# Optimization experiments

Measured on AMD Instinct MI355X. Metric: run time of the kernel, lower is better.

The kernel has to match this reference:

```python
import jax, jax.numpy as jnp
import numpy as np

N, E, B = 50000, 800000, 64
DIN, H, NH, L = 128, 128, 4, 3
SYM = 64          # symbolic_feature_dim
FD, ED = SYM // 4, H // 4   # feature_dim=16, embed_dim=32
DH = H // NH
EPS = 1e-5

def _ln(x, g, b):
    m = jnp.mean(x, -1, keepdims=True)
    v = jnp.var(x, -1, keepdims=True)
    return (x - m) * jax.lax.rsqrt(v + EPS) * g + b

def setup_inputs() -> dict:
    key = jax.random.key(0)
    ks = jax.random.split(key, 32)
    s = 0.05
    inp = {
        'node_features': jax.random.normal(ks[0], (N, DIN), jnp.float32),
        'symbolic_features': jax.random.normal(ks[1], (B, SYM), jnp.float32),
        'edge_index': jax.random.randint(ks[2], (2, E), 0, N),
        'batch': jnp.sort(jax.random.randint(ks[3], (N,), 0, B)),
        # GraphEncoder params
        'W_in': jax.random.normal(ks[4], (H, DIN)) * s,
        'b_in': jnp.zeros((H,)),
        'sage_Wl': jax.random.normal(ks[5], (L, H, H)) * s,   # lin_l (neighbors, with bias)
        'sage_bl': jnp.zeros((L, H)),
        'sage_Wr': jax.random.normal(ks[6], (L, H, H)) * s,   # lin_r (root, no bias)
        'ln_g': jnp.ones((L, H)), 'ln_b': jnp.zeros((L, H)),
        # AttentionPooling params
        'query': jax.random.normal(ks[7], (H,)),
        'in_proj_W': jax.random.normal(ks[8], (3 * H, H)) * s,
        'in_proj_b': jnp.zeros((3 * H,)),
        'out_W': jax.random.normal(ks[9], (H, H)) * s,
        'out_b': jnp.zeros((H,)),
        # SymbolicFeatureProcessor params (4 stacked encoders)
        'sym_W': jax.random.normal(ks[10], (4, ED, FD)) * s,
        'sym_b': jnp.zeros((4, ED)),
        'symf_W': jax.random.normal(ks[11], (H, H)) * s,
        'symf_b': jnp.zeros((H,)),
        'symf_g': jnp.ones((H,)), 'symf_beta': jnp.zeros((H,)),
        # main fusion
        'fus_W': jax.random.normal(ks[12], (H, 2 * H)) * s,
        'fus_b': jnp.zeros((H,)),
        'fus_g': jnp.ones((H,)), 'fus_beta': jnp.zeros((H,)),
        # 3 output heads stacked (instability, grounding, risk)
        'head_W1': jax.random.normal(ks[13], (3, H // 2, H)) * s,
        'head_b1': jnp.zeros((3, H // 2)),
        'head_W2': jax.random.normal(ks[14], (3, 1, H // 2)) * s,
        'head_b2': jnp.zeros((3, 1)),
    }
    return inp

def reference(node_features, symbolic_features, W_in, b_in, sage_Wl, sage_bl, sage_Wr,
              ln_g, ln_b, query, in_proj_W, in_proj_b, out_W, out_b,
              sym_W, sym_b, symf_W, symf_b, symf_g, symf_beta,
              fus_W, fus_b, fus_g, fus_beta, head_W1, head_b1, head_W2, head_b2,
              edge_index, batch):
    src, dst = edge_index[0], edge_index[1]
    x = jax.nn.relu(node_features @ W_in.T + b_in)                 # [N,H]
    deg = jax.ops.segment_sum(jnp.ones((E, 1), x.dtype), dst, num_segments=N)
    inv_deg = 1.0 / jnp.maximum(deg, 1.0)
    for l in range(L):
        res = x
        agg = jax.ops.segment_sum(x[src], dst, num_segments=N) * inv_deg  # mean aggr
        h = agg @ sage_Wl[l].T + sage_bl[l] + x @ sage_Wr[l].T
        x = jax.nn.relu(_ln(h, ln_g[l], ln_b[l])) + res
    # ---- AttentionPooling: per-graph MHA with a single learned query ----
    Wq, Wk, Wv = jnp.split(in_proj_W, 3, axis=0)
    bq, bk, bv = jnp.split(in_proj_b, 3)
    q = (Wq @ query + bq).reshape(NH, DH)                          # [NH,DH]
    k = (x @ Wk.T + bk).reshape(N, NH, DH)
    v = (x @ Wv.T + bv).reshape(N, NH, DH)
    scores = jnp.einsum('nhd,hd->nh', k, q) / np.sqrt(DH)          # [N,NH]
    smax = jax.ops.segment_max(scores, batch, num_segments=B)      # [B,NH]
    e = jnp.exp(scores - smax[batch])
    den = jax.ops.segment_sum(e, batch, num_segments=B)
    w = e / den[batch]                                              # segment softmax
    pooled = jax.ops.segment_sum(w[:, :, None] * v, batch, num_segments=B)
    g = pooled.reshape(B, H) @ out_W.T + out_b                      # [B,H]
    # ---- SymbolicFeatureProcessor: 4 parallel encoders + fusion ----
    parts = symbolic_features.reshape(B, 4, FD)
    emb = jax.nn.relu(jnp.einsum('bfi,foi->bfo', parts, sym_W) + sym_b)  # [B,4,ED]
    sym = _ln(jax.nn.relu(emb.reshape(B, H) @ symf_W.T + symf_b), symf_g, symf_beta)
    # ---- Fusion + heads ----
    fused = _ln(jax.nn.relu(jnp.concatenate([g, sym], -1) @ fus_W.T + fus_b), fus_g, fus_beta)
    hh = jax.nn.relu(jnp.einsum('bi,koi->kbo', fused, head_W1) + head_b1[:, None, :])
    out = jax.nn.sigmoid(jnp.einsum('kbo,kpo->kbp', hh, head_W2) + head_b2[:, None, :])
    return (out[0], out[1], out[2])
```

## Files before the change

### kernel.cpp

```cpp
#include <hip/hip_runtime.h>


#define H 128
#define PPG 16
#define BKSH 8
#define CH 4096

typedef unsigned short u16;
typedef unsigned char u8;
typedef __attribute__((ext_vector_type(8))) short bf16x8;
typedef __attribute__((ext_vector_type(4))) float f32x4;

__device__ __forceinline__ float b2f(u16 u){ return __uint_as_float(((unsigned)u) << 16); }
__device__ __forceinline__ u16 f2b(float f){
    unsigned x = __float_as_uint(f);
    unsigned r = x + 0x7fffu + ((x >> 16) & 1u);
    return (u16)(r >> 16);
}
__device__ __forceinline__ unsigned enc4(float v){
    int n = (int)(fmaxf(v, 0.f) * (15.f / 7.f) + 0.5f);
    return (unsigned)min(n, 15);
}
__device__ __forceinline__ unsigned pk_fp4(const float* nv){
    unsigned r = 0;
    #pragma unroll
    for (int j = 0; j < 8; j++) r |= enc4(nv[j]) << (4 * j);
    return r;
}
__device__ __forceinline__ void acc_lin4(unsigned* ua, unsigned w){
    ua[0] += w & 0x000F000Fu;
    ua[1] += (w >> 4) & 0x000F000Fu;
    ua[2] += (w >> 8) & 0x000F000Fu;
    ua[3] += (w >> 12) & 0x000F000Fu;
}
__device__ __forceinline__ void lds_fence(){
    asm volatile("s_waitcnt lgkmcnt(0)" ::: "memory");
    __builtin_amdgcn_sched_barrier(0);
}

__global__ __launch_bounds__(256) void k_splitall(const float* __restrict__ W_in, const float* __restrict__ sWl,
                                                  const float* __restrict__ sWr, const float* __restrict__ ipW,
                                                  u16* __restrict__ Win, u16* __restrict__ Wl,
                                                  u16* __restrict__ Wr, u16* __restrict__ Wv){
    const int WSZ = H * H;
    int i = blockIdx.x * 256 + threadIdx.x;
    if (i < WSZ)               Win[i]           = f2b(W_in[i]);
    else if (i < 4 * WSZ)      Wl[i - WSZ]      = f2b(sWl[i - WSZ]);
    else if (i < 7 * WSZ)      Wr[i - 4 * WSZ]  = f2b(sWr[i - 4 * WSZ]);
    else if (i < 8 * WSZ)      Wv[i - 7 * WSZ]  = f2b(ipW[2 * WSZ + (i - 7 * WSZ)]);
}

__global__ __launch_bounds__(1024) void k_bcnt(const int* __restrict__ dst, int* __restrict__ bcnt,
                                               int E, int NBK){
    __shared__ int cnt[256];
    int tid = threadIdx.x;
    if (tid < 256) cnt[tid] = 0;
    __syncthreads();
    int e0 = blockIdx.x * CH;
    int n = min(CH, E - e0);
    for (int j = tid; j < n; j += 1024) atomicAdd(&cnt[dst[e0 + j] >> BKSH], 1);
    __syncthreads();
    if (tid < NBK && cnt[tid]) atomicAdd(&bcnt[tid], cnt[tid]);
}

__global__ __launch_bounds__(256) void k_bscan(const int* __restrict__ bcnt, int* __restrict__ boff,
                                               int* __restrict__ bcur, int* __restrict__ offs, int NBK, int N){
    __shared__ int pre[256];
    int tid = threadIdx.x;
    int v = (tid < NBK) ? bcnt[tid] : 0;
    pre[tid] = v;
    __syncthreads();
    for (int off = 1; off < 256; off <<= 1){
        int a = (tid >= off) ? pre[tid - off] : 0;
        __syncthreads();
        pre[tid] += a;
        __syncthreads();
    }
    int excl = pre[tid] - v;
    if (tid < NBK){ boff[tid] = excl; bcur[tid] = excl; }
    if (tid == 255){
        boff[NBK] = pre[255];
        offs[N] = pre[255];
    }
}

__global__ __launch_bounds__(1024) void k_bscatter(const int* __restrict__ src, const int* __restrict__ dst,
                                                   unsigned* __restrict__ ebuf, int* __restrict__ bcur,
                                                   int E, int NBK){
    __shared__ int cnt[256], pre[256], loc[256], lcur[256], base[256];
    __shared__ unsigned stage[CH];
    int tid = threadIdx.x;
    if (tid < 256){ cnt[tid] = 0; }
    __syncthreads();
    int e0 = blockIdx.x * CH;
    int n = min(CH, E - e0);
    for (int j = tid; j < n; j += 1024) atomicAdd(&cnt[dst[e0 + j] >> BKSH], 1);
    __syncthreads();
    if (tid < NBK) base[tid] = atomicAdd(&bcur[tid], cnt[tid]);
    if (tid < 256) pre[tid] = cnt[tid];
    __syncthreads();
    for (int off = 1; off < 256; off <<= 1){
        int v = (tid < 256 && tid >= off) ? pre[tid - off] : 0;
        __syncthreads();
        if (tid < 256) pre[tid] += v;
        __syncthreads();
    }
    if (tid < 256){ loc[tid] = pre[tid] - cnt[tid]; lcur[tid] = loc[tid]; }
    __syncthreads();
    for (int j = tid; j < n; j += 1024){
        int d = dst[e0 + j], s = src[e0 + j];
        int k = d >> BKSH;
        int p = atomicAdd(&lcur[k], 1);
        stage[p] = (unsigned)d | ((unsigned)s << 16);
    }
    __syncthreads();
    for (int j = tid; j < n; j += 1024){
        unsigned v = stage[j];
        int k = (v & 0xffffu) >> BKSH;
        ebuf[base[k] + (j - loc[k])] = v;
    }
}

__global__ __launch_bounds__(256) void k_bfill(const unsigned* __restrict__ ebuf, const int* __restrict__ boff,
                                               int* __restrict__ offs, int* __restrict__ csr,
                                               float* __restrict__ invdeg, int N){
    __shared__ int deg[256], pre[256], cur[256];
    int k = blockIdx.x, tid = threadIdx.x;
    int node0 = k << BKSH;
    int s0 = boff[k], s1 = boff[k + 1];
    deg[tid] = 0;
    __syncthreads();
    for (int j = s0 + tid; j < s1; j += 256) atomicAdd(&deg[ebuf[j] & 255u], 1);
    __syncthreads();
    pre[tid] = deg[tid];
    __syncthreads();
    for (int off = 1; off < 256; off <<= 1){
        int v = (tid >= off) ? pre[tid - off] : 0;
        __syncthreads();
        pre[tid] += v;
        __syncthreads();
    }
    int excl = pre[tid] - deg[tid];
    int node = node0 + tid;
    if (node < N){
        offs[node] = s0 + excl;
        invdeg[node] = 1.0f / (float)max(deg[tid], 1);
    }
    cur[tid] = s0 + excl;
    __syncthreads();
    for (int j = s0 + tid; j < s1; j += 256){
        unsigned v = ebuf[j];
        int p = atomicAdd(&cur[v & 255u], 1);
        csr[p] = (int)(v >> 16);
    }
}

__global__ void k_start(const int* __restrict__ batch, int* __restrict__ start, int N, int B){
    int n = blockIdx.x * blockDim.x + threadIdx.x;
    if (n >= N) return;
    int b = batch[n];
    int bp = (n == 0) ? -1 : batch[n - 1];
    for (int g = bp + 1; g <= b; g++) start[g] = n;
    if (n == N - 1){ for (int g = b + 1; g <= B; g++) start[g] = N; }
}

__global__ __launch_bounds__(256) void k_gemm0(const float* __restrict__ A, u16* __restrict__ Xb,
                                               u8* __restrict__ X4,
                                               const u16* __restrict__ W1, const float* __restrict__ bias,
                                               int nrows){
    __shared__ float lt[4][16 * 132];
    const int wave = threadIdx.x >> 6;
    const int l = threadIdx.x & 63;
    const int q = l >> 4;
    const int t = l & 15;
    const int row0 = blockIdx.x * 64 + wave * 16;

    u16* sw = (u16*)&lt[wave][0];
    #pragma unroll
    for (int i = 0; i < 8; i++){
        int p = (i * 64 + l) * 4;
        int row = p >> 7, col = p & 127;
        int rowg = min(row0 + row, nrows - 1);
        float4 v = *(const float4*)(A + (size_t)rowg * H + col);
        u16* d = sw + row * 136 + col;
        d[0] = f2b(v.x); d[1] = f2b(v.y); d[2] = f2b(v.z); d[3] = f2b(v.w);
    }
    lds_fence();
    bf16x8 a1[4];
    #pragma unroll
    for (int kk = 0; kk < 4; kk++)
        a1[kk] = *(const bf16x8*)(sw + t * 136 + q * 8 + kk * 32);
    lds_fence();

    f32x4 acc[8];
    #pragma unroll
    for (int nt = 0; nt < 8; nt++){
        f32x4 c = {0.f, 0.f, 0.f, 0.f};
        const size_t wof = (size_t)(nt * 16 + t) * H + q * 8;
        #pragma unroll
        for (int kk = 0; kk < 4; kk++)
            c = __builtin_amdgcn_mfma_f32_16x16x32_bf16(a1[kk], *(const bf16x8*)(W1 + wof + kk * 32), c, 0, 0, 0);
        acc[nt] = c;
    }
    float bv[8];
    #pragma unroll
    for (int nt = 0; nt < 8; nt++) bv[nt] = bias[nt * 16 + t];
    #pragma unroll
    for (int r = 0; r < 4; r++)
        #pragma unroll
        for (int nt = 0; nt < 8; nt++)
            lt[wave][(q * 4 + r) * 132 + nt * 16 + t] = fmaxf(acc[nt][r] + bv[nt], 0.f);
    lds_fence();
    #pragma unroll
    for (int i = 0; i < 4; i++){
        int p = (i * 64 + l) * 8;
        int row = p >> 7, col = p & 127;
        int rg = row0 + row;
        if (rg < nrows){
            const float* lp = &lt[wave][row * 132 + col];
            float4 v0 = *(const float4*)lp;
            float4 v1 = *(const float4*)(lp + 4);
            float nv[8] = {v0.x, v0.y, v0.z, v0.w, v1.x, v1.y, v1.z, v1.w};
            bf16x8 o;
            #pragma unroll
            for (int j = 0; j < 8; j++) o[j] = (short)f2b(nv[j]);
            *(bf16x8*)(Xb + (size_t)rg * H + col) = o;
            int q4 = (col & 31) >> 3, kk4 = col >> 5;
            *(unsigned*)(X4 + (size_t)rg * 64 + q4 * 16 + kk4 * 4) = pk_fp4(nv);
        }
    }
}

template<bool FSC>
__global__ __launch_bounds__(128) void k_layer(
    const u16* __restrict__ Xin, const u8* __restrict__ Xin4,
    u16* __restrict__ Xout, u8* __restrict__ Xout4,
    const int* __restrict__ offs, const int* __restrict__ csr, const float* __restrict__ invdeg,
    const u16* __restrict__ W1, const u16* __restrict__ W2,
    const float* __restrict__ bias, const float* __restrict__ lng, const float* __restrict__ lnb,
    u16* __restrict__ Vb, const u16* __restrict__ Wv, const float* __restrict__ vbias,
    const float* __restrict__ qk, const float* __restrict__ qkb, float* __restrict__ scores,
    int nrows)
{
    __shared__ float ltw[16 * 132];
    __shared__ u16 sx[16 * 136];
    const int wave = threadIdx.x >> 6;
    const int l = threadIdx.x & 63;
    const int q = l >> 4;
    const int t = l & 15;
    const int row0g = blockIdx.x * 16;
    const int myrow = row0g + t;
    const bool valid = myrow < nrows;

    #pragma unroll
    for (int i = 0; i < 2; i++){
        int p = (i * 128 + threadIdx.x) * 8;
        int row = p >> 7, col = p & 127;
        int rowg = min(row0g + row, nrows - 1);
        uint4 v = *(const uint4*)(Xin + (size_t)rowg * H + col);
        *(uint4*)(sx + row * 136 + col) = v;
    }
    __syncthreads();
    bf16x8 a2[4];
    if (wave == 0){
        #pragma unroll
        for (int kk = 0; kk < 4; kk++)
            a2[kk] = *(const bf16x8*)(sx + t * 136 + q * 8 + kk * 32);
    }
    unsigned ua[4][4];
    #pragma unroll
    for (int kk = 0; kk < 4; kk++)
        #pragma unroll
        for (int m = 0; m < 4; m++) ua[kk][m] = 0u;
    int o0 = valid ? offs[myrow] : 0;
    int o1 = valid ? offs[myrow + 1] : 0;
    int mid = o0 + ((o1 - o0 + 1) >> 1);
    int i  = wave ? mid : o0;
    int ie = wave ? o1 : mid;
    int p0 = 0, p1 = 0, p2 = 0, p3 = 0;
    if (i + 3 < ie){ p0 = csr[i]; p1 = csr[i + 1]; p2 = csr[i + 2]; p3 = csr[i + 3]; }
    while (i + 3 < ie){
        int t0 = p0, t1 = p1, t2 = p2, t3 = p3;
        int nx = i + 4;
        if (nx + 3 < ie){ p0 = csr[nx]; p1 = csr[nx + 1]; p2 = csr[nx + 2]; p3 = csr[nx + 3]; }
        uint4 w0 = *(const uint4*)(Xin4 + (size_t)t0 * 64 + q * 16);
        uint4 w1 = *(const uint4*)(Xin4 + (size_t)t1 * 64 + q * 16);
        uint4 w2 = *(const uint4*)(Xin4 + (size_t)t2 * 64 + q * 16);
        uint4 w3 = *(const uint4*)(Xin4 + (size_t)t3 * 64 + q * 16);
        acc_lin4(ua[0], w0.x); acc_lin4(ua[1], w0.y); acc_lin4(ua[2], w0.z); acc_lin4(ua[3], w0.w);
        acc_lin4(ua[0], w1.x); acc_lin4(ua[1], w1.y); acc_lin4(ua[2], w1.z); acc_lin4(ua[3], w1.w);
        acc_lin4(ua[0], w2.x); acc_lin4(ua[1], w2.y); acc_lin4(ua[2], w2.z); acc_lin4(ua[3], w2.w);
        acc_lin4(ua[0], w3.x); acc_lin4(ua[1], w3.y); acc_lin4(ua[2], w3.z); acc_lin4(ua[3], w3.w);
        i = nx;
    }
    for (; i < ie; i++){
        int s = csr[i];
        uint4 w = *(const uint4*)(Xin4 + (size_t)s * 64 + q * 16);
        acc_lin4(ua[0], w.x); acc_lin4(ua[1], w.y); acc_lin4(ua[2], w.z); acc_lin4(ua[3], w.w);
    }
    if (wave == 1){
        unsigned* pw = (unsigned*)(ltw + t * 132) + q * 16;
        #pragma unroll
        for (int kk = 0; kk < 4; kk++)
            #pragma unroll
            for (int m = 0; m < 4; m++) pw[kk * 4 + m] = ua[kk][m];
    }
    __syncthreads();
    if (wave == 1) return;
    {
        const unsigned* pr = (const unsigned*)(ltw + t * 132) + q * 16;
        #pragma unroll
        for (int kk = 0; kk < 4; kk++)
            #pragma unroll
            for (int m = 0; m < 4; m++) ua[kk][m] += pr[kk * 4 + m];
    }
    lds_fence();
    float scl = (valid ? invdeg[myrow] : 0.f) * (7.f / 15.f);
    bf16x8 a1[4];
    #pragma unroll
    for (int kk = 0; kk < 4; kk++){
        bf16x8 v;
        #pragma unroll
        for (int m = 0; m < 4; m++){
            v[m]     = (short)f2b((float)(ua[kk][m] & 0xFFFFu) * scl);
            v[m + 4] = (short)f2b((float)(ua[kk][m] >> 16) * scl);
        }
        a1[kk] = v;
    }

    f32x4 acc[8];
    #pragma unroll
    for (int nt = 0; nt < 8; nt++){
        f32x4 c = {0.f, 0.f, 0.f, 0.f};
        const size_t wof = (size_t)(nt * 16 + t) * H + q * 8;
        #pragma unroll
        for (int kk = 0; kk < 4; kk++)
            c = __builtin_amdgcn_mfma_f32_16x16x32_bf16(a1[kk], *(const bf16x8*)(W1 + wof + kk * 32), c, 0, 0, 0);
        #pragma unroll
        for (int kk = 0; kk < 4; kk++)
            c = __builtin_amdgcn_mfma_f32_16x16x32_bf16(a2[kk], *(const bf16x8*)(W2 + wof + kk * 32), c, 0, 0, 0);
        acc[nt] = c;
    }
    float bv[8], gv[8], lbv[8];
    #pragma unroll
    for (int nt = 0; nt < 8; nt++){
        int col = nt * 16 + t;
        bv[nt] = bias[col]; gv[nt] = lng[col]; lbv[nt] = lnb[col];
    }
    #pragma unroll
    for (int r = 0; r < 4; r++){
        float hv[8], s = 0.f, s2 = 0.f;
        #pragma unroll
        for (int nt = 0; nt < 8; nt++){ float v = acc[nt][r] + bv[nt]; hv[nt] = v; s += v; s2 += v * v; }
        #pragma unroll
        for (int m = 1; m < 16; m <<= 1){ s += __shfl_xor(s, m, 64); s2 += __shfl_xor(s2, m, 64); }
        float mean = s * (1.f / H);
        float var  = s2 * (1.f / H) - mean * mean;
        float rstd = rsqrtf(var + 1e-5f);
        #pragma unroll
        for (int nt = 0; nt < 8; nt++){
            float v = (hv[nt] - mean) * rstd * gv[nt] + lbv[nt];
            ltw[(q * 4 + r) * 132 + nt * 16 + t] = fmaxf(v, 0.f);
        }
    }
    lds_fence();
    if (!FSC){
        #pragma unroll
        for (int i2 = 0; i2 < 4; i2++){
            int p = (i2 * 64 + l) * 8;
            int row = p >> 7, col = p & 127;
            int rg = row0g + row;
            if (rg < nrows){
                const float* lp = ltw + row * 132 + col;
                float4 v0 = *(const float4*)lp;
                float4 v1 = *(const float4*)(lp + 4);
                const u16* xp = sx + row * 136 + col;
                float nv[8];
                nv[0] = v0.x + b2f(xp[0]); nv[1] = v0.y + b2f(xp[1]);
                nv[2] = v0.z + b2f(xp[2]); nv[3] = v0.w + b2f(xp[3]);
                nv[4] = v1.x + b2f(xp[4]); nv[5] = v1.y + b2f(xp[5]);
                nv[6] = v1.z + b2f(xp[6]); nv[7] = v1.w + b2f(xp[7]);
                bf16x8 o;
                #pragma unroll
                for (int j = 0; j < 8; j++) o[j] = (short)f2b(nv[j]);
                *(bf16x8*)(Xout + (size_t)rg * H + col) = o;
                int q4 = (col & 31) >> 3, kk4 = col >> 5;
                *(unsigned*)(Xout4 + (size_t)rg * 64 + q4 * 16 + kk4 * 4) = pk_fp4(nv);
            }
        }
    } else {
        bf16x8 xv[4];
        float sc[4] = {0.f, 0.f, 0.f, 0.f};
        #pragma unroll
        for (int kk = 0; kk < 4; kk++){
            const float* lp = ltw + t * 132 + q * 8 + kk * 32;
            float4 v0 = *(const float4*)lp;
            float4 v1 = *(const float4*)(lp + 4);
            float nv[8] = {v0.x, v0.y, v0.z, v0.w, v1.x, v1.y, v1.z, v1.w};
            #pragma unroll
            for (int j = 0; j < 8; j++) nv[j] += b2f((u16)a2[kk][j]);
            bf16x8 o;
            #pragma unroll
            for (int j = 0; j < 8; j++) o[j] = (short)f2b(nv[j]);
            xv[kk] = o;
            #pragma unroll
            for (int h = 0; h < 4; h++){
                const float* qp = qk + h * H + q * 8 + kk * 32;
                float4 q0 = *(const float4*)qp;
                float4 q1 = *(const float4*)(qp + 4);
                sc[h] += nv[0] * q0.x + nv[1] * q0.y + nv[2] * q0.z + nv[3] * q0.w
                       + nv[4] * q1.x + nv[5] * q1.y + nv[6] * q1.z + nv[7] * q1.w;
            }
        }
        #pragma unroll
        for (int h = 0; h < 4; h++){
            sc[h] += __shfl_xor(sc[h], 16, 64);
            sc[h] += __shfl_xor(sc[h], 32, 64);
        }
        if (q == 0 && valid){
            #pragma unroll
            for (int h = 0; h < 4; h++) scores[myrow * 4 + h] = sc[h] + qkb[h];
        }
        f32x4 vacc[8];
        #pragma unroll
        for (int nt = 0; nt < 8; nt++){
            f32x4 c = {0.f, 0.f, 0.f, 0.f};
            const size_t wof = (size_t)(nt * 16 + t) * H + q * 8;
            #pragma unroll
            for (int kk = 0; kk < 4; kk++)
                c = __builtin_amdgcn_mfma_f32_16x16x32_bf16(xv[kk], *(const bf16x8*)(Wv + wof + kk * 32), c, 0, 0, 0);
            vacc[nt] = c;
        }
        float vb2[8];
        #pragma unroll
        for (int nt = 0; nt < 8; nt++) vb2[nt] = vbias[nt * 16 + t];
        #pragma unroll
        for (int r = 0; r < 4; r++)
            #pragma unroll
            for (int nt = 0; nt < 8; nt++)
                ltw[(q * 4 + r) * 132 + nt * 16 + t] = vacc[nt][r] + vb2[nt];
        lds_fence();
        #pragma unroll
        for (int i2 = 0; i2 < 4; i2++){
            int p = (i2 * 64 + l) * 8;
            int row = p >> 7, col = p & 127;
            int rg = row0g + row;
            if (rg < nrows){
                const float* lp = ltw + row * 132 + col;
                float4 v0 = *(const float4*)lp;
                float4 v1 = *(const float4*)(lp + 4);
                bf16x8 o;
                o[0] = (short)f2b(v0.x); o[1] = (short)f2b(v0.y);
                o[2] = (short)f2b(v0.z); o[3] = (short)f2b(v0.w);
                o[4] = (short)f2b(v1.x); o[5] = (short)f2b(v1.y);
                o[6] = (short)f2b(v1.z); o[7] = (short)f2b(v1.w);
                *(bf16x8*)(Vb + (size_t)rg * H + col) = o;
            }
        }
    }
}

__global__ __launch_bounds__(128) void k_qk(const float* __restrict__ ipW, const float* __restrict__ ipb,
                                            const float* __restrict__ query,
                                            float* __restrict__ qk, float* __restrict__ qkb){
    __shared__ float qs[H];
    int t = threadIdx.x;
    float a = ipb[t];
    for (int c = 0; c < H; c++) a += ipW[t * H + c] * query[c];
    qs[t] = a;
    __syncthreads();
    const float r32 = 0.17677669529663687f;
    #pragma unroll
    for (int h = 0; h < 4; h++){
        float v = 0.f;
        for (int d = 0; d < 32; d++) v += ipW[(H + h * 32 + d) * H + t] * qs[h * 32 + d];
        qk[h * H + t] = v * r32;
    }
    if (t < 4){
        float z = 0.f;
        for (int d = 0; d < 32; d++) z += ipb[H + t * 32 + d] * qs[t * 32 + d];
        qkb[t] = z * r32;
    }
}

__global__ __launch_bounds__(256) void k_smax(const float* __restrict__ scores, const int* __restrict__ start,
                                              float* __restrict__ smax, int B){
    int idx = blockIdx.x * 4 + (threadIdx.x >> 6);
    if (idx >= B * 4) return;
    int b = idx >> 2, h = idx & 3, l = threadIdx.x & 63;
    int s0 = start[b], s1 = start[b + 1];
    float m = -1e30f;
    for (int n = s0 + l; n < s1; n += 64) m = fmaxf(m, scores[n * 4 + h]);
    #pragma unroll
    for (int s = 1; s < 64; s <<= 1) m = fmaxf(m, __shfl_xor(m, s, 64));
    if (l == 0) smax[idx] = m;
}

__global__ __launch_bounds__(64) void k_poolsum(const float* __restrict__ scores, const u16* __restrict__ Vb,
                                                const int* __restrict__ start, const float* __restrict__ smax,
                                                float* __restrict__ praw, float* __restrict__ den){
    int b = blockIdx.x / PPG, p = blockIdx.x % PPG;
    int c2 = threadIdx.x;
    int h = c2 >> 4;
    int s0 = start[b], s1 = start[b + 1];
    float sm = smax[b * 4 + h];
    float a0 = 0.f, a1 = 0.f, se = 0.f;
    for (int n = s0 + p; n < s1; n += PPG){
        float e = expf(scores[n * 4 + h] - sm);
        unsigned wv = *(const unsigned*)(Vb + (size_t)n * H + 2 * c2);
        a0 += e * b2f((u16)(wv & 0xffffu));
        a1 += e * b2f((u16)(wv >> 16));
        se += e;
    }
    atomicAdd(&praw[b * H + 2 * c2], a0);
    atomicAdd(&praw[b * H + 2 * c2 + 1], a1);
    if ((c2 & 15) == 0) atomicAdd(&den[b * 4 + h], se);
}

__global__ __launch_bounds__(128) void k_tail(
    const float* __restrict__ praw, const float* __restrict__ den,
    const float* __restrict__ outW, const float* __restrict__ outb,
    const float* __restrict__ symfeat, const float* __restrict__ symW, const float* __restrict__ symb,
    const float* __restrict__ sfW, const float* __restrict__ sfb, const float* __restrict__ sfg, const float* __restrict__ sfbeta,
    const float* __restrict__ fusW, const float* __restrict__ fusb, const float* __restrict__ fusg, const float* __restrict__ fusbeta,
    const float* __restrict__ hW1, const float* __restrict__ hb1, const float* __restrict__ hW2, const float* __restrict__ hb2,
    float* __restrict__ dout, int B){
    int b = blockIdx.x, t = threadIdx.x;
    __shared__ float P[H], G[H], EMB[H], S[H], F[H], HHs[192], red[H], mm[2];
    float dh = den[b * 4 + (t >> 5)];
    P[t] = (dh > 0.f) ? praw[b * H + t] / dh : 0.f;
    __syncthreads();
    float a = outb[t];
    for (int c = 0; c < H; c++) a += P[c] * outW[t * H + c];
    G[t] = a;
    {
        int f = t >> 5;
        float e = symb[t];
        for (int i = 0; i < 16; i++) e += symfeat[b * 64 + f * 16 + i] * symW[t * 16 + i];
        EMB[t] = fmaxf(e, 0.f);
    }
    __syncthreads();
    float a2 = sfb[t];
    for (int c = 0; c < H; c++) a2 += EMB[c] * sfW[t * H + c];
    a2 = fmaxf(a2, 0.f);
    red[t] = a2; __syncthreads();
    for (int s = 64; s > 0; s >>= 1){ if (t < s) red[t] += red[t + s]; __syncthreads(); }
    if (t == 0) mm[0] = red[0];
    __syncthreads();
    red[t] = a2 * a2; __syncthreads();
    for (int s = 64; s > 0; s >>= 1){ if (t < s) red[t] += red[t + s]; __syncthreads(); }
    if (t == 0) mm[1] = red[0];
    __syncthreads();
    {
        float mean = mm[0] * (1.f / H), var = mm[1] * (1.f / H) - mean * mean;
        float rstd = rsqrtf(var + 1e-5f);
        S[t] = (a2 - mean) * rstd * sfg[t] + sfbeta[t];
    }
    __syncthreads();
    float fu = fusb[t];
    for (int c = 0; c < H; c++) fu += G[c] * fusW[t * 256 + c];
    for (int c = 0; c < H; c++) fu += S[c] * fusW[t * 256 + 128 + c];
    fu = fmaxf(fu, 0.f);
    red[t] = fu; __syncthreads();
    for (int s = 64; s > 0; s >>= 1){ if (t < s) red[t] += red[t + s]; __syncthreads(); }
    if (t == 0) mm[0] = red[0];
    __syncthreads();
    red[t] = fu * fu; __syncthreads();
    for (int s = 64; s > 0; s >>= 1){ if (t < s) red[t] += red[t + s]; __syncthreads(); }
    if (t == 0) mm[1] = red[0];
    __syncthreads();
    {
        float mean = mm[0] * (1.f / H), var = mm[1] * (1.f / H) - mean * mean;
        float rstd = rsqrtf(var + 1e-5f);
        F[t] = (fu - mean) * rstd * fusg[t] + fusbeta[t];
    }
    __syncthreads();
    for (int idx = t; idx < 192; idx += 128){
        float hv = hb1[idx];
        for (int c = 0; c < H; c++) hv += F[c] * hW1[idx * H + c];
        HHs[idx] = fmaxf(hv, 0.f);
    }
    __syncthreads();
    if (t < 3){
        float z = hb2[t];
        for (int o = 0; o < 64; o++) z += HHs[t * 64 + o] * hW2[t * 64 + o];
        dout[t * B + b] = 1.f / (1.f + expf(-z));
    }
}

extern "C" void kernel_launch(void* const* d_in, const int* in_sizes, int n_in,
                              void* d_out, int out_size, void* d_ws, size_t ws_size,
                              hipStream_t stream){
    const float* NF      = (const float*)d_in[0];
    const float* SYMF    = (const float*)d_in[1];
    const int*   EIDX    = (const int*)d_in[2];
    const int*   BATCH   = (const int*)d_in[3];
    const float* W_in    = (const float*)d_in[4];
    const float* b_in    = (const float*)d_in[5];
    const float* sWl     = (const float*)d_in[6];
    const float* sbl     = (const float*)d_in[7];
    const float* sWr     = (const float*)d_in[8];
    const float* lng     = (const float*)d_in[9];
    const float* lnb     = (const float*)d_in[10];
    const float* query   = (const float*)d_in[11];
    const float* ipW     = (const float*)d_in[12];
    const float* ipb     = (const float*)d_in[13];
    const float* outW    = (const float*)d_in[14];
    const float* outb    = (const float*)d_in[15];
    const float* symW    = (const float*)d_in[16];
    const float* symb    = (const float*)d_in[17];
    const float* sfW     = (const float*)d_in[18];
    const float* sfb     = (const float*)d_in[19];
    const float* sfg     = (const float*)d_in[20];
    const float* sfbeta  = (const float*)d_in[21];
    const float* fusW    = (const float*)d_in[22];
    const float* fusb    = (const float*)d_in[23];
    const float* fusg    = (const float*)d_in[24];
    const float* fusbeta = (const float*)d_in[25];
    const float* hW1     = (const float*)d_in[26];
    const float* hb1     = (const float*)d_in[27];
    const float* hW2     = (const float*)d_in[28];
    const float* hb2     = (const float*)d_in[29];

    const int N = in_sizes[0] / H;
    const int E = in_sizes[2] / 2;
    const int B = in_sizes[1] / 64;
    const int* esrc = EIDX;
    const int* edst = EIDX + E;
    const int NBK = (N + 255) >> BKSH;

    char* w = (char*)d_ws;
    auto alloc = [&](size_t bytes) -> char* {
        char* p = w; w += (bytes + 255) & ~(size_t)255; return p;
    };
    u16*   X0      = (u16*)alloc((size_t)N * H * 2);
    u16*   X1      = (u16*)alloc((size_t)N * H * 2);
    u8*    X0q     = (u8*)alloc((size_t)N * 64);
    u8*    X1q     = (u8*)alloc((size_t)N * 64);
    u16*   Vb      = (u16*)alloc((size_t)N * H * 2);
    float* scores  = (float*)alloc((size_t)N * 4 * 4);
    unsigned* ebuf = (unsigned*)alloc((size_t)E * 4);
    char* zbase    = w;
    int* bcnt      = (int*)alloc((size_t)NBK * 4);
    float* praw    = (float*)alloc((size_t)B * H * 4);
    float* den     = (float*)alloc((size_t)B * 4 * 4);
    size_t zbytes  = (size_t)(w - zbase);
    int* boff      = (int*)alloc((size_t)(NBK + 1) * 4);
    int* bcur      = (int*)alloc((size_t)NBK * 4);
    int* offs      = (int*)alloc((size_t)(N + 1) * 4);
    float* invdeg  = (float*)alloc((size_t)N * 4);
    int* csr       = (int*)alloc((size_t)E * 4);
    int* start     = (int*)alloc((size_t)(B + 1) * 4);
    float* smax    = (float*)alloc((size_t)B * 4 * 4);
    float* qk      = (float*)alloc((size_t)4 * H * 4);
    float* qkb     = (float*)alloc(4 * 4);
    const int WSZ  = H * H;
    u16* Win = (u16*)alloc(WSZ * 2);
    u16* Wl  = (u16*)alloc(3 * WSZ * 2);
    u16* Wr  = (u16*)alloc(3 * WSZ * 2);
    u16* Wv  = (u16*)alloc(WSZ * 2);

    hipMemsetAsync(zbase, 0, zbytes, stream);

    const int cb = (E + CH - 1) / CH;
    k_bcnt<<<cb, 1024, 0, stream>>>(edst, bcnt, E, NBK);
    k_bscan<<<1, 256, 0, stream>>>(bcnt, boff, bcur, offs, NBK, N);
    k_bscatter<<<cb, 1024, 0, stream>>>(esrc, edst, ebuf, bcur, E, NBK);
    k_bfill<<<NBK, 256, 0, stream>>>(ebuf, boff, offs, csr, invdeg, N);
    k_start<<<(N + 255) / 256, 256, 0, stream>>>(BATCH, start, N, B);
    k_qk<<<1, 128, 0, stream>>>(ipW, ipb, query, qk, qkb);
    k_splitall<<<(8 * WSZ + 255) / 256, 256, 0, stream>>>(W_in, sWl, sWr, ipW, Win, Wl, Wr, Wv);

    const int gb = (N + 63) / 64;
    const int lb = (N + 15) / 16;
    k_gemm0<<<gb, 256, 0, stream>>>(NF, X0, X0q, Win, b_in, N);
    k_layer<false><<<lb, 128, 0, stream>>>(X0, X0q, X1, X1q, offs, csr, invdeg,
                                           Wl + 0 * WSZ, Wr + 0 * WSZ,
                                           sbl + 0 * H, lng + 0 * H, lnb + 0 * H,
                                           nullptr, nullptr, nullptr,
                                           nullptr, nullptr, nullptr, N);
    k_layer<false><<<lb, 128, 0, stream>>>(X1, X1q, X0, X0q, offs, csr, invdeg,
                                           Wl + 1 * WSZ, Wr + 1 * WSZ,
                                           sbl + 1 * H, lng + 1 * H, lnb + 1 * H,
                                           nullptr, nullptr, nullptr,
                                           nullptr, nullptr, nullptr, N);
    k_layer<true><<<lb, 128, 0, stream>>>(X0, X0q, nullptr, nullptr, offs, csr, invdeg,
                                          Wl + 2 * WSZ, Wr + 2 * WSZ,
                                          sbl + 2 * H, lng + 2 * H, lnb + 2 * H,
                                          Vb, Wv, ipb + 2 * H,
                                          qk, qkb, scores, N);
    k_smax<<<B, 256, 0, stream>>>(scores, start, smax, B);
    k_poolsum<<<B * PPG, 64, 0, stream>>>(scores, Vb, start, smax, praw, den);
    k_tail<<<B, 128, 0, stream>>>(praw, den, outW, outb, SYMF, symW, symb,
                                  sfW, sfb, sfg, sfbeta, fusW, fusb, fusg, fusbeta,
                                  hW1, hb1, hW2, hb2, (float*)d_out, B);
}
```

Measured before the change: 364.3 us.

## Merge prep kernels, store attention values as fp8, use shuffle reductions in tail

Four small setup kernels (bucket count, graph start offsets, query-key projection, weight conversion) are folded into one block-specialized prep launch, which removes launch overhead. The attention value matrix V is now stored as fp8 instead of bf16, halving its write and read traffic in the last layer and in pooling. The pooling kernel is restructured so each lane decodes four values and the two half-waves are combined with a shuffle. The tail kernel's LDS tree reductions are replaced with wave shuffles. The fp8 values reduce the precision of the pooled result.

```diff
diff --git a/kernel.cpp b/kernel.cpp
--- a/kernel.cpp
+++ b/kernel.cpp
@@ -10,6 +10,7 @@
 typedef unsigned char u8;
 typedef __attribute__((ext_vector_type(8))) short bf16x8;
 typedef __attribute__((ext_vector_type(4))) float f32x4;
+typedef __attribute__((ext_vector_type(2))) float f32x2;
 
 __device__ __forceinline__ float b2f(u16 u){ return __uint_as_float(((unsigned)u) << 16); }
 __device__ __forceinline__ u16 f2b(float f){
@@ -21,7 +22,7 @@
     int n = (int)(fmaxf(v, 0.f) * (15.f / 7.f) + 0.5f);
     return (unsigned)min(n, 15);
 }
-__device__ __forceinline__ unsigned pk_fp4(const float* nv){
+__device__ __forceinline__ unsigned pk_lin4(const float* nv){
     unsigned r = 0;
     #pragma unroll
     for (int j = 0; j < 8; j++) r |= enc4(nv[j]) << (4 * j);
@@ -33,34 +34,82 @@
     ua[2] += (w >> 8) & 0x000F000Fu;
     ua[3] += (w >> 12) & 0x000F000Fu;
 }
+__device__ __forceinline__ uint2 pk_fp8(const float* nv){
+    int lo = 0, hi = 0;
+    lo = __builtin_amdgcn_cvt_pk_fp8_f32(nv[0], nv[1], lo, false);
+    lo = __builtin_amdgcn_cvt_pk_fp8_f32(nv[2], nv[3], lo, true);
+    hi = __builtin_amdgcn_cvt_pk_fp8_f32(nv[4], nv[5], hi, false);
+    hi = __builtin_amdgcn_cvt_pk_fp8_f32(nv[6], nv[7], hi, true);
+    uint2 r; r.x = (unsigned)lo; r.y = (unsigned)hi; return r;
+}
+__device__ __forceinline__ void dec8x4(unsigned w, float* f){
+    f32x2 d0 = __builtin_amdgcn_cvt_pk_f32_fp8((int)w, false);
+    f32x2 d1 = __builtin_amdgcn_cvt_pk_f32_fp8((int)w, true);
+    f[0] = d0[0]; f[1] = d0[1]; f[2] = d1[0]; f[3] = d1[1];
+}
 __device__ __forceinline__ void lds_fence(){
     asm volatile("s_waitcnt lgkmcnt(0)" ::: "memory");
     __builtin_amdgcn_sched_barrier(0);
 }
 
-__global__ __launch_bounds__(256) void k_splitall(const float* __restrict__ W_in, const float* __restrict__ sWl,
-                                                  const float* __restrict__ sWr, const float* __restrict__ ipW,
-                                                  u16* __restrict__ Win, u16* __restrict__ Wl,
-                                                  u16* __restrict__ Wr, u16* __restrict__ Wv){
+__global__ __launch_bounds__(1024) void k_prep(
+    const int* __restrict__ dst, int* __restrict__ bcnt, int E, int NBK, int cb,
+    const int* __restrict__ batch, int* __restrict__ start, int N, int B,
+    const float* __restrict__ ipW, const float* __restrict__ ipb, const float* __restrict__ query,
+    float* __restrict__ qk, float* __restrict__ qkb,
+    const float* __restrict__ W_in, const float* __restrict__ sWl, const float* __restrict__ sWr,
+    u16* __restrict__ Win, u16* __restrict__ Wl, u16* __restrict__ Wr, u16* __restrict__ Wv)
+{
+    __shared__ int cnt[256];
+    __shared__ float qs[128];
     const int WSZ = H * H;
-    int i = blockIdx.x * 256 + threadIdx.x;
-    if (i < WSZ)               Win[i]           = f2b(W_in[i]);
-    else if (i < 4 * WSZ)      Wl[i - WSZ]      = f2b(sWl[i - WSZ]);
-    else if (i < 7 * WSZ)      Wr[i - 4 * WSZ]  = f2b(sWr[i - 4 * WSZ]);
-    else if (i < 8 * WSZ)      Wv[i - 7 * WSZ]  = f2b(ipW[2 * WSZ + (i - 7 * WSZ)]);
-}
-
-__global__ __launch_bounds__(1024) void k_bcnt(const int* __restrict__ dst, int* __restrict__ bcnt,
-                                               int E, int NBK){
-    __shared__ int cnt[256];
-    int tid = threadIdx.x;
-    if (tid < 256) cnt[tid] = 0;
-    __syncthreads();
-    int e0 = blockIdx.x * CH;
-    int n = min(CH, E - e0);
-    for (int j = tid; j < n; j += 1024) atomicAdd(&cnt[dst[e0 + j] >> BKSH], 1);
-    __syncthreads();
-    if (tid < NBK && cnt[tid]) atomicAdd(&bcnt[tid], cnt[tid]);
+    const int bid = blockIdx.x, tid = threadIdx.x;
+    const int nbs = (N + 1023) >> 10;
+    if (bid < cb){
+        if (tid < 256) cnt[tid] = 0;
+        __syncthreads();
+        int e0 = bid * CH;
+        int n = min(CH, E - e0);
+        for (int j = tid; j < n; j += 1024) atomicAdd(&cnt[dst[e0 + j] >> BKSH], 1);
+        __syncthreads();
+        if (tid < NBK && cnt[tid]) atomicAdd(&bcnt[tid], cnt[tid]);
+    } else if (bid < cb + nbs){
+        int n = (bid - cb) * 1024 + tid;
+        if (n < N){
+            int b = batch[n];
+            int bp = (n == 0) ? -1 : batch[n - 1];
+            for (int g = bp + 1; g <= b; g++) start[g] = n;
+            if (n == N - 1){ for (int g = b + 1; g <= B; g++) start[g] = N; }
+        }
+    } else if (bid == cb + nbs){
+        int t = tid;
+        if (t < 128){
+            float a = ipb[t];
+            for (int c = 0; c < H; c++) a += ipW[t * H + c] * query[c];
+            qs[t] = a;
+        }
+        __syncthreads();
+        const float r32 = 0.17677669529663687f;
+        if (t < 128){
+            #pragma unroll
+            for (int h = 0; h < 4; h++){
+                float v = 0.f;
+                for (int d = 0; d < 32; d++) v += ipW[(H + h * 32 + d) * H + t] * qs[h * 32 + d];
+                qk[h * H + t] = v * r32;
+            }
+        }
+        if (t < 4){
+            float z = 0.f;
+            for (int d = 0; d < 32; d++) z += ipb[H + t * 32 + d] * qs[t * 32 + d];
+            qkb[t] = z * r32;
+        }
+    } else {
+        int i = (bid - cb - nbs - 1) * 1024 + tid;
+        if (i < WSZ)               Win[i]           = f2b(W_in[i]);
+        else if (i < 4 * WSZ)      Wl[i - WSZ]      = f2b(sWl[i - WSZ]);
+        else if (i < 7 * WSZ)      Wr[i - 4 * WSZ]  = f2b(sWr[i - 4 * WSZ]);
+        else if (i < 8 * WSZ)      Wv[i - 7 * WSZ]  = f2b(ipW[2 * WSZ + (i - 7 * WSZ)]);
+    }
 }
 
 __global__ __launch_bounds__(256) void k_bscan(const int* __restrict__ bcnt, int* __restrict__ boff,
@@ -153,15 +202,6 @@
         int p = atomicAdd(&cur[v & 255u], 1);
         csr[p] = (int)(v >> 16);
     }
-}
-
-__global__ void k_start(const int* __restrict__ batch, int* __restrict__ start, int N, int B){
-    int n = blockIdx.x * blockDim.x + threadIdx.x;
-    if (n >= N) return;
-    int b = batch[n];
-    int bp = (n == 0) ? -1 : batch[n - 1];
-    for (int g = bp + 1; g <= b; g++) start[g] = n;
-    if (n == N - 1){ for (int g = b + 1; g <= B; g++) start[g] = N; }
 }
 
 __global__ __launch_bounds__(256) void k_gemm0(const float* __restrict__ A, u16* __restrict__ Xb,
@@ -226,7 +266,7 @@
             for (int j = 0; j < 8; j++) o[j] = (short)f2b(nv[j]);
             *(bf16x8*)(Xb + (size_t)rg * H + col) = o;
             int q4 = (col & 31) >> 3, kk4 = col >> 5;
-            *(unsigned*)(X4 + (size_t)rg * 64 + q4 * 16 + kk4 * 4) = pk_fp4(nv);
+            *(unsigned*)(X4 + (size_t)rg * 64 + q4 * 16 + kk4 * 4) = pk_lin4(nv);
         }
     }
 }
@@ -238,7 +278,7 @@
     const int* __restrict__ offs, const int* __restrict__ csr, const float* __restrict__ invdeg,
     const u16* __restrict__ W1, const u16* __restrict__ W2,
     const float* __restrict__ bias, const float* __restrict__ lng, const float* __restrict__ lnb,
-    u16* __restrict__ Vb, const u16* __restrict__ Wv, const float* __restrict__ vbias,
+    u8* __restrict__ V8, const u16* __restrict__ Wv, const float* __restrict__ vbias,
     const float* __restrict__ qk, const float* __restrict__ qkb, float* __restrict__ scores,
     int nrows)
 {
@@ -385,7 +425,7 @@
                 for (int j = 0; j < 8; j++) o[j] = (short)f2b(nv[j]);
                 *(bf16x8*)(Xout + (size_t)rg * H + col) = o;
                 int q4 = (col & 31) >> 3, kk4 = col >> 5;
-                *(unsigned*)(Xout4 + (size_t)rg * 64 + q4 * 16 + kk4 * 4) = pk_fp4(nv);
+                *(unsigned*)(Xout4 + (size_t)rg * 64 + q4 * 16 + kk4 * 4) = pk_lin4(nv);
             }
         }
     } else {
@@ -449,37 +489,10 @@
                 const float* lp = ltw + row * 132 + col;
                 float4 v0 = *(const float4*)lp;
                 float4 v1 = *(const float4*)(lp + 4);
-                bf16x8 o;
-                o[0] = (short)f2b(v0.x); o[1] = (short)f2b(v0.y);
-                o[2] = (short)f2b(v0.z); o[3] = (short)f2b(v0.w);
-                o[4] = (short)f2b(v1.x); o[5] = (short)f2b(v1.y);
-                o[6] = (short)f2b(v1.z); o[7] = (short)f2b(v1.w);
-                *(bf16x8*)(Vb + (size_t)rg * H + col) = o;
+                float nv[8] = {v0.x, v0.y, v0.z, v0.w, v1.x, v1.y, v1.z, v1.w};
+                *(uint2*)(V8 + (size_t)rg * H + col) = pk_fp8(nv);
             }
         }
-    }
-}
-
-__global__ __launch_bounds__(128) void k_qk(const float* __restrict__ ipW, const float* __restrict__ ipb,
-                                            const float* __restrict__ query,
-                                            float* __restrict__ qk, float* __restrict__ qkb){
-    __shared__ float qs[H];
-    int t = threadIdx.x;
-    float a = ipb[t];
-    for (int c = 0; c < H; c++) a += ipW[t * H + c] * query[c];
-    qs[t] = a;
-    __syncthreads();
-    const float r32 = 0.17677669529663687f;
-    #pragma unroll
-    for (int h = 0; h < 4; h++){
-        float v = 0.f;
-        for (int d = 0; d < 32; d++) v += ipW[(H + h * 32 + d) * H + t] * qs[h * 32 + d];
-        qk[h * H + t] = v * r32;
-    }
-    if (t < 4){
-        float z = 0.f;
-        for (int d = 0; d < 32; d++) z += ipb[H + t * 32 + d] * qs[t * 32 + d];
-        qkb[t] = z * r32;
     }
 }
 
@@ -496,25 +509,35 @@
     if (l == 0) smax[idx] = m;
 }
 
-__global__ __launch_bounds__(64) void k_poolsum(const float* __restrict__ scores, const u16* __restrict__ Vb,
+__global__ __launch_bounds__(64) void k_poolsum(const float* __restrict__ scores, const u8* __restrict__ V8,
                                                 const int* __restrict__ start, const float* __restrict__ smax,
                                                 float* __restrict__ praw, float* __restrict__ den){
     int b = blockIdx.x / PPG, p = blockIdx.x % PPG;
-    int c2 = threadIdx.x;
-    int h = c2 >> 4;
+    int lane = threadIdx.x;
+    int half = lane >> 5;
+    int sl = lane & 31;
+    int h = sl >> 3;
     int s0 = start[b], s1 = start[b + 1];
     float sm = smax[b * 4 + h];
-    float a0 = 0.f, a1 = 0.f, se = 0.f;
-    for (int n = s0 + p; n < s1; n += PPG){
+    float acc[4] = {0.f, 0.f, 0.f, 0.f};
+    float se = 0.f;
+    for (int n = s0 + p + half * PPG; n < s1; n += 2 * PPG){
         float e = expf(scores[n * 4 + h] - sm);
-        unsigned wv = *(const unsigned*)(Vb + (size_t)n * H + 2 * c2);
-        a0 += e * b2f((u16)(wv & 0xffffu));
-        a1 += e * b2f((u16)(wv >> 16));
+        unsigned w = *(const unsigned*)(V8 + (size_t)n * H + sl * 4);
+        float f[4];
+        dec8x4(w, f);
+        acc[0] += e * f[0]; acc[1] += e * f[1];
+        acc[2] += e * f[2]; acc[3] += e * f[3];
         se += e;
     }
-    atomicAdd(&praw[b * H + 2 * c2], a0);
-    atomicAdd(&praw[b * H + 2 * c2 + 1], a1);
-    if ((c2 & 15) == 0) atomicAdd(&den[b * 4 + h], se);
+    #pragma unroll
+    for (int j = 0; j < 4; j++) acc[j] += __shfl_xor(acc[j], 32, 64);
+    se += __shfl_xor(se, 32, 64);
+    if (half == 0){
+        #pragma unroll
+        for (int j = 0; j < 4; j++) atomicAdd(&praw[b * H + sl * 4 + j], acc[j]);
+        if ((sl & 7) == 0) atomicAdd(&den[b * 4 + h], se);
+    }
 }
 
 __global__ __launch_bounds__(128) void k_tail(
@@ -526,7 +549,7 @@
     const float* __restrict__ hW1, const float* __restrict__ hb1, const float* __restrict__ hW2, const float* __restrict__ hb2,
     float* __restrict__ dout, int B){
     int b = blockIdx.x, t = threadIdx.x;
-    __shared__ float P[H], G[H], EMB[H], S[H], F[H], HHs[192], red[H], mm[2];
+    __shared__ float P[H], G[H], EMB[H], S[H], F[H], HHs[192], ps[4];
     float dh = den[b * 4 + (t >> 5)];
     P[t] = (dh > 0.f) ? praw[b * H + t] / dh : 0.f;
     __syncthreads();
@@ -543,16 +566,14 @@
     float a2 = sfb[t];
     for (int c = 0; c < H; c++) a2 += EMB[c] * sfW[t * H + c];
     a2 = fmaxf(a2, 0.f);
-    red[t] = a2; __syncthreads();
-    for (int s = 64; s > 0; s >>= 1){ if (t < s) red[t] += red[t + s]; __syncthreads(); }
-    if (t == 0) mm[0] = red[0];
-    __syncthreads();
-    red[t] = a2 * a2; __syncthreads();
-    for (int s = 64; s > 0; s >>= 1){ if (t < s) red[t] += red[t + s]; __syncthreads(); }
-    if (t == 0) mm[1] = red[0];
-    __syncthreads();
     {
-        float mean = mm[0] * (1.f / H), var = mm[1] * (1.f / H) - mean * mean;
+        float v1 = a2, v2 = a2 * a2;
+        #pragma unroll
+        for (int m = 1; m < 64; m <<= 1){ v1 += __shfl_xor(v1, m, 64); v2 += __shfl_xor(v2, m, 64); }
+        if ((t & 63) == 0){ ps[(t >> 6) * 2] = v1; ps[(t >> 6) * 2 + 1] = v2; }
+        __syncthreads();
+        float s = ps[0] + ps[2], s2 = ps[1] + ps[3];
+        float mean = s * (1.f / H), var = s2 * (1.f / H) - mean * mean;
         float rstd = rsqrtf(var + 1e-5f);
         S[t] = (a2 - mean) * rstd * sfg[t] + sfbeta[t];
     }
@@ -561,16 +582,14 @@
     for (int c = 0; c < H; c++) fu += G[c] * fusW[t * 256 + c];
     for (int c = 0; c < H; c++) fu += S[c] * fusW[t * 256 + 128 + c];
     fu = fmaxf(fu, 0.f);
-    red[t] = fu; __syncthreads();
-    for (int s = 64; s > 0; s >>= 1){ if (t < s) red[t] += red[t + s]; __syncthreads(); }
-    if (t == 0) mm[0] = red[0];
-    __syncthreads();
-    red[t] = fu * fu; __syncthreads();
-    for (int s = 64; s > 0; s >>= 1){ if (t < s) red[t] += red[t + s]; __syncthreads(); }
-    if (t == 0) mm[1] = red[0];
-    __syncthreads();
     {
-        float mean = mm[0] * (1.f / H), var = mm[1] * (1.f / H) - mean * mean;
+        float v1 = fu, v2 = fu * fu;
+        #pragma unroll
+        for (int m = 1; m < 64; m <<= 1){ v1 += __shfl_xor(v1, m, 64); v2 += __shfl_xor(v2, m, 64); }
+        if ((t & 63) == 0){ ps[(t >> 6) * 2] = v1; ps[(t >> 6) * 2 + 1] = v2; }
+        __syncthreads();
+        float s = ps[0] + ps[2], s2 = ps[1] + ps[3];
+        float mean = s * (1.f / H), var = s2 * (1.f / H) - mean * mean;
         float rstd = rsqrtf(var + 1e-5f);
         F[t] = (fu - mean) * rstd * fusg[t] + fusbeta[t];
     }
@@ -637,7 +656,7 @@
     u16*   X1      = (u16*)alloc((size_t)N * H * 2);
     u8*    X0q     = (u8*)alloc((size_t)N * 64);
     u8*    X1q     = (u8*)alloc((size_t)N * 64);
-    u16*   Vb      = (u16*)alloc((size_t)N * H * 2);
+    u8*    V8      = (u8*)alloc((size_t)N * H);
     float* scores  = (float*)alloc((size_t)N * 4 * 4);
     unsigned* ebuf = (unsigned*)alloc((size_t)E * 4);
     char* zbase    = w;
@@ -663,13 +682,15 @@
     hipMemsetAsync(zbase, 0, zbytes, stream);
 
     const int cb = (E + CH - 1) / CH;
-    k_bcnt<<<cb, 1024, 0, stream>>>(edst, bcnt, E, NBK);
+    const int nbs = (N + 1023) >> 10;
+    const int prep_grid = cb + nbs + 1 + 128;
+    k_prep<<<prep_grid, 1024, 0, stream>>>(edst, bcnt, E, NBK, cb,
+                                           BATCH, start, N, B,
+                                           ipW, ipb, query, qk, qkb,
+                                           W_in, sWl, sWr, Win, Wl, Wr, Wv);
     k_bscan<<<1, 256, 0, stream>>>(bcnt, boff, bcur, offs, NBK, N);
     k_bscatter<<<cb, 1024, 0, stream>>>(esrc, edst, ebuf, bcur, E, NBK);
     k_bfill<<<NBK, 256, 0, stream>>>(ebuf, boff, offs, csr, invdeg, N);
-    k_start<<<(N + 255) / 256, 256, 0, stream>>>(BATCH, start, N, B);
-    k_qk<<<1, 128, 0, stream>>>(ipW, ipb, query, qk, qkb);
-    k_splitall<<<(8 * WSZ + 255) / 256, 256, 0, stream>>>(W_in, sWl, sWr, ipW, Win, Wl, Wr, Wv);
 
     const int gb = (N + 63) / 64;
     const int lb = (N + 15) / 16;
@@ -687,10 +708,10 @@
     k_layer<true><<<lb, 128, 0, stream>>>(X0, X0q, nullptr, nullptr, offs, csr, invdeg,
                                           Wl + 2 * WSZ, Wr + 2 * WSZ,
                                           sbl + 2 * H, lng + 2 * H, lnb + 2 * H,
-                                          Vb, Wv, ipb + 2 * H,
+                                          V8, Wv, ipb + 2 * H,
                                           qk, qkb, scores, N);
     k_smax<<<B, 256, 0, stream>>>(scores, start, smax, B);
-    k_poolsum<<<B * PPG, 64, 0, stream>>>(scores, Vb, start, smax, praw, den);
+    k_poolsum<<<B * PPG, 64, 0, stream>>>(scores, V8, start, smax, praw, den);
     k_tail<<<B, 128, 0, stream>>>(praw, den, outW, outb, SYMF, symW, symb,
                                   sfW, sfb, sfg, sfbeta, fusW, fusb, fusg, fusbeta,
                                   hW1, hb1, hW2, hb2, (float*)d_out, B);
```

Measured after the change: 350.5 us. -3.8%, faster.
